# Kernel optimization log

Hardware: AMD Instinct MI355X
Metric: run time of the kernel (lower is better)

Reference implementation:

```python
import jax, jax.numpy as jnp
import numpy as np

N = 50000      # nodes
E = 800000     # edges
IN = 128       # in_channels
H = 128        # hidden_channels
OUT = 500      # out_channels
EPS = 1e-5


def setup_inputs() -> dict:
    key = jax.random.key(0)
    ks = jax.random.split(key, 8)
    def rn(k, shape, scale=0.05):
        return jax.random.normal(k, shape, jnp.float32) * scale
    return {
        "x": jax.random.normal(ks[0], (N, IN), jnp.float32),
        "edge_index": jax.random.randint(ks[1], (2, E), 0, N, dtype=jnp.int32),
        "W1": rn(ks[2], (IN, H)), "b1": jnp.zeros((H,), jnp.float32),
        "g1": jnp.ones((H,), jnp.float32), "be1": jnp.zeros((H,), jnp.float32),
        "W2": rn(ks[3], (H, 2 * H)), "b2": jnp.zeros((2 * H,), jnp.float32),
        "g2": jnp.ones((2 * H,), jnp.float32), "be2": jnp.zeros((2 * H,), jnp.float32),
        "W3": rn(ks[4], (2 * H, H)), "b3": jnp.zeros((H,), jnp.float32),
        "g3": jnp.ones((H,), jnp.float32), "be3": jnp.zeros((H,), jnp.float32),
        "Wl1": rn(ks[5], (H, H // 2)), "bl1": jnp.zeros((H // 2,), jnp.float32),
        "g4": jnp.ones((H // 2,), jnp.float32), "be4": jnp.zeros((H // 2,), jnp.float32),
        "Wl2": rn(ks[6], (H // 2, OUT)), "bl2": jnp.zeros((OUT,), jnp.float32),
    }


def layer_norm(x, g, b):
    mu = jnp.mean(x, axis=-1, keepdims=True)
    var = jnp.mean(jnp.square(x - mu), axis=-1, keepdims=True)
    return (x - mu) * jax.lax.rsqrt(var + EPS) * g + b


def gcn_conv(x, W, b, src, dst, n):
    # PyG GCNConv: x' = D^{-1/2} (A + I) D^{-1/2} (x W) + b, with self-loops.
    h = x @ W                                   # [N, F]
    ones = jnp.ones(src.shape[0], h.dtype)
    deg = jax.ops.segment_sum(ones, dst, num_segments=n) + 1.0  # +1 self-loop
    dinv = jnp.where(deg > 0, jax.lax.rsqrt(deg), 0.0)          # [N]
    coef = dinv[src] * dinv[dst]                # [E]
    agg = jax.ops.segment_sum(h[src] * coef[:, None], dst, num_segments=n)
    agg = agg + h * jnp.square(dinv)[:, None]   # self-loop messages
    return agg + b


def reference(x, edge_index, W1, b1, g1, be1, W2, b2, g2, be2,
              W3, b3, g3, be3, Wl1, bl1, g4, be4, Wl2, bl2):
    # eval mode: dropout is identity
    src, dst = edge_index[0], edge_index[1]
    n = x.shape[0]
    h = jax.nn.elu(layer_norm(gcn_conv(x, W1, b1, src, dst, n), g1, be1))
    h = jax.nn.elu(layer_norm(gcn_conv(h, W2, b2, src, dst, n), g2, be2))
    h = jax.nn.elu(layer_norm(gcn_conv(h, W3, b3, src, dst, n), g3, be3))
    h = jax.nn.elu(layer_norm(h @ Wl1 + bl1, g4, be4))
    return h @ Wl2 + bl2
```

## Files before the change

### kernel.cpp

```cpp
#include <hip/hip_runtime.h>
#include <cstdint>


#define LN_EPS 1e-5f

typedef __attribute__((ext_vector_type(8))) short bf16x8;
typedef __attribute__((ext_vector_type(4))) float f32x4;

static __device__ __forceinline__ ushort f2bf(float f) {
  union { float f; uint u; } c; c.f = f;
  uint u = c.u;
  return (ushort)((u + 0x7fffu + ((u >> 16) & 1u)) >> 16);
}
static __device__ __forceinline__ float bf2f(ushort h) {
  union { uint u; float f; } c; c.u = (uint)h << 16;
  return c.f;
}


__global__ void deg_kernel(const int* __restrict__ dst, int* __restrict__ deg, int E) {
  int e = blockIdx.x * blockDim.x + threadIdx.x;
  if (e < E) atomicAdd(&deg[dst[e]], 1);
}

__global__ void scan1_kernel(const int* __restrict__ deg, int* __restrict__ excl,
                             int* __restrict__ bsums, float* __restrict__ dinv, int N) {
  __shared__ int s[256];
  int tid = threadIdx.x;
  int i = blockIdx.x * 256 + tid;
  int v = (i < N) ? deg[i] : 0;
  s[tid] = v;
  __syncthreads();
  for (int o = 1; o < 256; o <<= 1) {
    int t = (tid >= o) ? s[tid - o] : 0;
    __syncthreads();
    if (tid >= o) s[tid] += t;
    __syncthreads();
  }
  if (i < N) {
    excl[i] = s[tid] - v;
    dinv[i] = rsqrtf((float)v + 1.0f);
  }
  if (tid == 255) bsums[blockIdx.x] = s[tid];
}

__global__ void scan23_kernel(int* __restrict__ rowptr, int* __restrict__ fill,
                              const int* __restrict__ bsums, int N, int Etotal, int nb) {
  __shared__ int sh[256];
  const int tid = threadIdx.x;
  const int bix = blockIdx.x;
  int v = (tid < bix && tid < nb) ? bsums[tid] : 0;
  sh[tid] = v;
  __syncthreads();
  for (int o = 128; o > 0; o >>= 1) {
    if (tid < o) sh[tid] += sh[tid + o];
    __syncthreads();
  }
  const int off = sh[0];
  int i = bix * 256 + tid;
  if (i < N) {
    int r = rowptr[i] + off;
    rowptr[i] = r;
    fill[i] = r;
  } else if (i == N) {
    rowptr[N] = Etotal;
  }
}

__global__ void fill_kernel(const int* __restrict__ src, const int* __restrict__ dst,
                            int* __restrict__ fill, int* __restrict__ srcs, int E) {
  int e = blockIdx.x * blockDim.x + threadIdx.x;
  if (e >= E) return;
  int idx = atomicAdd(&fill[dst[e]], 1);
  srcs[idx] = src[e];
}


struct WConvArgs {
  const float* w[5];
  ushort* wt[5];
  int K[5], N[5];
  int off[6];
};

__global__ void prep_kernel(WConvArgs a, int total, int* __restrict__ deg, int Nn) {
  int i = blockIdx.x * blockDim.x + threadIdx.x;
  if (i < Nn) deg[i] = 0;
  if (i < 768) a.wt[4][32000 + i] = 0;
  if (i >= total) return;
  int m = 0;
  while (i >= a.off[m + 1]) m++;
  int j = i - a.off[m];
  int k = j / a.N[m], n = j - k * a.N[m];
  a.wt[m][(size_t)n * a.K[m] + k] = f2bf(a.w[m][j]);
}

#define TBM 128
#define TBN 128
#define TBK 32
#define LDK 40

template <int AF32>
__global__ __launch_bounds__(256, 2) void mfma_gemm_kernel(
    const void* __restrict__ A, const ushort* __restrict__ Bt,
    const float* __restrict__ bias, ushort* __restrict__ Cout,
    int M, int N, int K) {
  __shared__ ushort As[TBM][LDK];
  __shared__ ushort Bs[TBN][LDK];
  const int tid = threadIdx.x;
  const int lane = tid & 63;
  const int w = tid >> 6;
  const int wm = w & 1, wn = w >> 1;
  const int quad = lane >> 4, l16 = lane & 15;
  const int rowBase = blockIdx.y * TBM;
  const int colBase = blockIdx.x * TBN;

  f32x4 acc[4][4] = {};
  const int lr = tid >> 2;
  const int lk = (tid & 3) * 8;

  for (int k0 = 0; k0 < K; k0 += TBK) {
#pragma unroll
    for (int h = 0; h < 2; h++) {
      int r = lr + h * 64;
      int grow = rowBase + r;
      if (AF32) {
        const float* Af = (const float*)A;
        float4 v0 = make_float4(0.f, 0.f, 0.f, 0.f), v1 = v0;
        if (grow < M) {
          const float* ap = Af + (size_t)grow * K + k0 + lk;
          v0 = *(const float4*)ap;
          v1 = *(const float4*)(ap + 4);
        }
        uint4 wv;
        wv.x = (uint)f2bf(v0.x) | ((uint)f2bf(v0.y) << 16);
        wv.y = (uint)f2bf(v0.z) | ((uint)f2bf(v0.w) << 16);
        wv.z = (uint)f2bf(v1.x) | ((uint)f2bf(v1.y) << 16);
        wv.w = (uint)f2bf(v1.z) | ((uint)f2bf(v1.w) << 16);
        *(uint4*)&As[r][lk] = wv;
      } else {
        const ushort* Ab = (const ushort*)A;
        uint4 va = make_uint4(0, 0, 0, 0);
        if (grow < M) va = *(const uint4*)(Ab + (size_t)grow * K + k0 + lk);
        *(uint4*)&As[r][lk] = va;
      }
      int gcol = colBase + r;
      uint4 vb = make_uint4(0, 0, 0, 0);
      if (gcol < N) vb = *(const uint4*)(Bt + (size_t)gcol * K + k0 + lk);
      *(uint4*)&Bs[r][lk] = vb;
    }
    __syncthreads();
    bf16x8 af[4], bfr[4];
#pragma unroll
    for (int i = 0; i < 4; i++) {
      af[i]  = *(const bf16x8*)&As[wm * 64 + i * 16 + l16][quad * 8];
      bfr[i] = *(const bf16x8*)&Bs[wn * 64 + i * 16 + l16][quad * 8];
    }
#pragma unroll
    for (int i = 0; i < 4; i++)
#pragma unroll
      for (int j = 0; j < 4; j++)
        acc[i][j] = __builtin_amdgcn_mfma_f32_16x16x32_bf16(af[i], bfr[j], acc[i][j], 0, 0, 0);
    __syncthreads();
  }
#pragma unroll
  for (int i = 0; i < 4; i++) {
    int row0 = rowBase + wm * 64 + i * 16 + quad * 4;
#pragma unroll
    for (int j = 0; j < 4; j++) {
      int col = colBase + wn * 64 + j * 16 + l16;
      if (col >= N) continue;
      float bv = bias ? bias[col] : 0.f;
#pragma unroll
      for (int r = 0; r < 4; r++) {
        int row = row0 + r;
        if (row >= M) continue;
        Cout[(size_t)row * N + col] = f2bf(acc[i][j][r] + bv);
      }
    }
  }
}

__global__ __launch_bounds__(256) void l4_kernel(
    const ushort* __restrict__ A, const ushort* __restrict__ Bt1,
    const float* __restrict__ bias1, const float* __restrict__ gamma,
    const float* __restrict__ beta, ushort* __restrict__ Hout, int M) {
  const int tid = threadIdx.x;
  const int lane = tid & 63;
  const int w = tid >> 6;
  const int quad = lane >> 4, l16 = lane & 15;
  const int rowBase = blockIdx.x * 64 + w * 16;

  bf16x8 bfr[4][4];
#pragma unroll
  for (int j = 0; j < 4; j++)
#pragma unroll
    for (int kk = 0; kk < 4; kk++)
      bfr[j][kk] = *(const bf16x8*)(Bt1 + (size_t)(j * 16 + l16) * 128 + kk * 32 + quad * 8);

  const int arow = rowBase + l16;
  bf16x8 af[4] = {};
  if (arow < M) {
#pragma unroll
    for (int kk = 0; kk < 4; kk++)
      af[kk] = *(const bf16x8*)(A + (size_t)arow * 128 + kk * 32 + quad * 8);
  }

  f32x4 acc[4] = {};
#pragma unroll
  for (int j = 0; j < 4; j++)
#pragma unroll
    for (int kk = 0; kk < 4; kk++)
      acc[j] = __builtin_amdgcn_mfma_f32_16x16x32_bf16(af[kk], bfr[j][kk], acc[j], 0, 0, 0);

#pragma unroll
  for (int r = 0; r < 4; r++) {
    float v[4];
    float s = 0.f;
#pragma unroll
    for (int j = 0; j < 4; j++) {
      v[j] = acc[j][r] + bias1[j * 16 + l16];
      s += v[j];
    }
#pragma unroll
    for (int o = 8; o >= 1; o >>= 1) s += __shfl_xor(s, o, 16);
    float mean = s * (1.0f / 64.0f);
    float q = 0.f;
#pragma unroll
    for (int j = 0; j < 4; j++) {
      float d = v[j] - mean;
      q += d * d;
    }
#pragma unroll
    for (int o = 8; o >= 1; o >>= 1) q += __shfl_xor(q, o, 16);
    float rstd = rsqrtf(q * (1.0f / 64.0f) + LN_EPS);
    int grow = rowBase + quad * 4 + r;
    if (grow < M) {
#pragma unroll
      for (int j = 0; j < 4; j++) {
        int col = j * 16 + l16;
        float y = (v[j] - mean) * rstd * gamma[col] + beta[col];
        y = (y > 0.f) ? y : expm1f(y);
        Hout[(size_t)grow * 64 + col] = f2bf(y);
      }
    }
  }
}

__global__ __launch_bounds__(256, 4) void l5_kernel(
    const ushort* __restrict__ H, const ushort* __restrict__ Bt2,
    const float* __restrict__ bias2, float* __restrict__ Cout, int M) {
  __shared__ ushort h4s[16][68];
  __shared__ __align__(16) float sout[16][500];
  const int tid = threadIdx.x;
  const int lane = tid & 63;
  const int w = tid >> 6;
  const int quad = lane >> 4, l16 = lane & 15;
  const int rowBase = blockIdx.x * 16;

  if (tid < 128) {
    int r = tid >> 3, c8 = (tid & 7) * 8;
    int grow = rowBase + r;
    uint4 v = make_uint4(0, 0, 0, 0);
    if (grow < M) v = *(const uint4*)(H + (size_t)grow * 64 + c8);
    *(uint4*)&h4s[r][c8] = v;
  }

  bf16x8 breg[8][2];
  float bvreg[8];
#pragma unroll
  for (int c = 0; c < 8; c++) {
    const int bcol = (w * 8 + c) * 16 + l16;
    breg[c][0] = *(const bf16x8*)(Bt2 + (size_t)bcol * 64 + quad * 8);
    breg[c][1] = *(const bf16x8*)(Bt2 + (size_t)bcol * 64 + 32 + quad * 8);
    bvreg[c] = (bcol < 500) ? bias2[bcol] : 0.f;
  }
  __syncthreads();

  bf16x8 a0 = *(const bf16x8*)&h4s[l16][quad * 8];
  bf16x8 a1 = *(const bf16x8*)&h4s[l16][quad * 8 + 32];
#pragma unroll
  for (int c = 0; c < 8; c++) {
    f32x4 pacc = {0.f, 0.f, 0.f, 0.f};
    pacc = __builtin_amdgcn_mfma_f32_16x16x32_bf16(a0, breg[c][0], pacc, 0, 0, 0);
    pacc = __builtin_amdgcn_mfma_f32_16x16x32_bf16(a1, breg[c][1], pacc, 0, 0, 0);
    const int col = (w * 8 + c) * 16 + l16;
    if (col < 500) {
#pragma unroll
      for (int r = 0; r < 4; r++)
        sout[quad * 4 + r][col] = pacc[r] + bvreg[c];
    }
  }
  __syncthreads();

#pragma unroll
  for (int k = 0; k < 8; k++) {
    int idx = k * 256 + tid;
    if (idx < 2000) {
      int r = idx / 125;
      int c4 = idx - r * 125;
      int grow = rowBase + r;
      if (grow < M) {
        float4 v = *(float4*)&sout[r][c4 * 4];
        *(float4*)&Cout[(size_t)grow * 500 + c4 * 4] = v;
      }
    }
  }
}


static __device__ __forceinline__ void acc8(float* a, uint4 v, float c) {
  a[0] += c * bf2f((ushort)(v.x & 0xffffu)); a[1] += c * bf2f((ushort)(v.x >> 16));
  a[2] += c * bf2f((ushort)(v.y & 0xffffu)); a[3] += c * bf2f((ushort)(v.y >> 16));
  a[4] += c * bf2f((ushort)(v.z & 0xffffu)); a[5] += c * bf2f((ushort)(v.z >> 16));
  a[6] += c * bf2f((ushort)(v.w & 0xffffu)); a[7] += c * bf2f((ushort)(v.w >> 16));
}

__global__ __launch_bounds__(256) void agg_kernel(
    const ushort* __restrict__ hb, const int* __restrict__ rowptr,
    const int* __restrict__ srcs, const float* __restrict__ dinv,
    uint* __restrict__ out, int Nn) {
  const int wave = threadIdx.x >> 6;
  const int n = blockIdx.x * 4 + wave;
  if (n >= Nn) return;
  const int lane = threadIdx.x & 63;
  const int g = lane >> 4, l16 = lane & 15;
  const uint4* h4 = (const uint4*)hb;
  const float di = dinv[n];
  float a[8] = {0.f, 0.f, 0.f, 0.f, 0.f, 0.f, 0.f, 0.f};
  if (g == 0) {
    uint4 sv = h4[(size_t)n * 16 + l16];
    acc8(a, sv, di * di);
  }
  int i = rowptr[n] + g;
  const int e = rowptr[n + 1];
  for (; i + 4 < e; i += 8) {
    int s0 = srcs[i], s1 = srcs[i + 4];
    float c0 = dinv[s0] * di, c1 = dinv[s1] * di;
    uint4 v0 = h4[(size_t)s0 * 16 + l16];
    uint4 v1 = h4[(size_t)s1 * 16 + l16];
    acc8(a, v0, c0);
    acc8(a, v1, c1);
  }
  if (i < e) {
    int s = srcs[i];
    float c = dinv[s] * di;
    uint4 v = h4[(size_t)s * 16 + l16];
    acc8(a, v, c);
  }
#pragma unroll
  for (int k = 0; k < 8; k++) {
    a[k] += __shfl_xor(a[k], 16);
    a[k] += __shfl_xor(a[k], 32);
  }
  if (g == 0) {
    uint4 o;
    o.x = (uint)f2bf(a[0]) | ((uint)f2bf(a[1]) << 16);
    o.y = (uint)f2bf(a[2]) | ((uint)f2bf(a[3]) << 16);
    o.z = (uint)f2bf(a[4]) | ((uint)f2bf(a[5]) << 16);
    o.w = (uint)f2bf(a[6]) | ((uint)f2bf(a[7]) << 16);
    ((uint4*)out)[(size_t)n * 16 + l16] = o;
  }
}

__global__ __launch_bounds__(256) void agg_ln_kernel(
    const ushort* __restrict__ hb, const int* __restrict__ rowptr,
    const int* __restrict__ srcs, const float* __restrict__ dinv,
    const float* __restrict__ bias, const float* __restrict__ gamma,
    const float* __restrict__ beta, uint* __restrict__ out, int Nn) {
  const int wave = threadIdx.x >> 6;
  const int n = blockIdx.x * 4 + wave;
  if (n >= Nn) return;
  const int lane = threadIdx.x & 63;
  const int g = lane >> 4, l16 = lane & 15;
  const uint4* h4 = (const uint4*)hb;
  const float di = dinv[n];
  float a[8] = {0.f, 0.f, 0.f, 0.f, 0.f, 0.f, 0.f, 0.f};
  if (g == 0) {
    uint4 sv = h4[(size_t)n * 16 + l16];
    acc8(a, sv, di * di);
    float4 b0 = ((const float4*)bias)[l16 * 2];
    float4 b1 = ((const float4*)bias)[l16 * 2 + 1];
    a[0] += b0.x; a[1] += b0.y; a[2] += b0.z; a[3] += b0.w;
    a[4] += b1.x; a[5] += b1.y; a[6] += b1.z; a[7] += b1.w;
  }
  int i = rowptr[n] + g;
  const int e = rowptr[n + 1];
  for (; i + 4 < e; i += 8) {
    int s0 = srcs[i], s1 = srcs[i + 4];
    float c0 = dinv[s0] * di, c1 = dinv[s1] * di;
    uint4 v0 = h4[(size_t)s0 * 16 + l16];
    uint4 v1 = h4[(size_t)s1 * 16 + l16];
    acc8(a, v0, c0);
    acc8(a, v1, c1);
  }
  if (i < e) {
    int s = srcs[i];
    float c = dinv[s] * di;
    uint4 v = h4[(size_t)s * 16 + l16];
    acc8(a, v, c);
  }
#pragma unroll
  for (int k = 0; k < 8; k++) {
    a[k] += __shfl_xor(a[k], 16);
    a[k] += __shfl_xor(a[k], 32);
  }
  float s = ((a[0] + a[1]) + (a[2] + a[3])) + ((a[4] + a[5]) + (a[6] + a[7]));
  s += __shfl_xor(s, 8);
  s += __shfl_xor(s, 4);
  s += __shfl_xor(s, 2);
  s += __shfl_xor(s, 1);
  float mean = s * (1.0f / 128.0f);
  float q = 0.f;
#pragma unroll
  for (int k = 0; k < 8; k++) {
    float d = a[k] - mean;
    q += d * d;
  }
  q += __shfl_xor(q, 8);
  q += __shfl_xor(q, 4);
  q += __shfl_xor(q, 2);
  q += __shfl_xor(q, 1);
  float rstd = rsqrtf(q * (1.0f / 128.0f) + LN_EPS);
  if (g == 0) {
    float4 g0 = ((const float4*)gamma)[l16 * 2];
    float4 g1 = ((const float4*)gamma)[l16 * 2 + 1];
    float4 e0 = ((const float4*)beta)[l16 * 2];
    float4 e1 = ((const float4*)beta)[l16 * 2 + 1];
    float gv[8] = {g0.x, g0.y, g0.z, g0.w, g1.x, g1.y, g1.z, g1.w};
    float ev[8] = {e0.x, e0.y, e0.z, e0.w, e1.x, e1.y, e1.z, e1.w};
    float y[8];
#pragma unroll
    for (int k = 0; k < 8; k++) {
      float t = (a[k] - mean) * rstd * gv[k] + ev[k];
      y[k] = (t > 0.f) ? t : expm1f(t);
    }
    uint4 o;
    o.x = (uint)f2bf(y[0]) | ((uint)f2bf(y[1]) << 16);
    o.y = (uint)f2bf(y[2]) | ((uint)f2bf(y[3]) << 16);
    o.z = (uint)f2bf(y[4]) | ((uint)f2bf(y[5]) << 16);
    o.w = (uint)f2bf(y[6]) | ((uint)f2bf(y[7]) << 16);
    ((uint4*)out)[(size_t)n * 16 + l16] = o;
  }
}

template <int F, bool IN_BF16>
__global__ __launch_bounds__(F) void ln_elu_kernel(const void* __restrict__ xin,
                                                   const float* __restrict__ g,
                                                   const float* __restrict__ be,
                                                   ushort* __restrict__ out) {
  constexpr int NW = (F + 63) / 64;
  __shared__ float sb[NW];
  const int row = blockIdx.x;
  const int f = threadIdx.x;
  float v;
  if (IN_BF16) v = bf2f(((const ushort*)xin)[(size_t)row * F + f]);
  else         v = ((const float*)xin)[(size_t)row * F + f];
  float s = v;
#pragma unroll
  for (int o = 32; o >= 1; o >>= 1) s += __shfl_xor(s, o);
  float mean;
  if constexpr (NW == 1) {
    mean = s * (1.0f / F);
  } else {
    if ((f & 63) == 0) sb[f >> 6] = s;
    __syncthreads();
    float t = 0.f;
#pragma unroll
    for (int w2 = 0; w2 < NW; w2++) t += sb[w2];
    mean = t * (1.0f / F);
    __syncthreads();
  }
  float d = v - mean;
  float q = d * d;
#pragma unroll
  for (int o = 32; o >= 1; o >>= 1) q += __shfl_xor(q, o);
  float var;
  if constexpr (NW == 1) {
    var = q * (1.0f / F);
  } else {
    if ((f & 63) == 0) sb[f >> 6] = q;
    __syncthreads();
    float t = 0.f;
#pragma unroll
    for (int w2 = 0; w2 < NW; w2++) t += sb[w2];
    var = t * (1.0f / F);
  }
  float y = d * rsqrtf(var + LN_EPS) * g[f] + be[f];
  out[(size_t)row * F + f] = f2bf((y > 0.f) ? y : expm1f(y));
}


extern "C" void kernel_launch(void* const* d_in, const int* in_sizes, int n_in,
                              void* d_out, int out_size, void* d_ws, size_t ws_size,
                              hipStream_t stream) {
  const float* x   = (const float*)d_in[0];
  const int*   ei  = (const int*)d_in[1];
  const float* W1  = (const float*)d_in[2];
  const float* b1  = (const float*)d_in[3];
  const float* g1  = (const float*)d_in[4];
  const float* be1 = (const float*)d_in[5];
  const float* W2  = (const float*)d_in[6];
  const float* b2  = (const float*)d_in[7];
  const float* g2  = (const float*)d_in[8];
  const float* be2 = (const float*)d_in[9];
  const float* W3  = (const float*)d_in[10];
  const float* b3  = (const float*)d_in[11];
  const float* g3  = (const float*)d_in[12];
  const float* be3 = (const float*)d_in[13];
  const float* Wl1 = (const float*)d_in[14];
  const float* bl1 = (const float*)d_in[15];
  const float* g4  = (const float*)d_in[16];
  const float* be4 = (const float*)d_in[17];
  const float* Wl2 = (const float*)d_in[18];
  const float* bl2 = (const float*)d_in[19];

  const int N = in_sizes[0] / 128;
  const int E = in_sizes[1] / 2;
  const int* esrc = ei;
  const int* edst = ei + E;

  char* p = (char*)d_ws;
  ushort* Pb = (ushort*)p;            p += (size_t)N * 256 * 2;
  ushort* Qb = (ushort*)p;            p += (size_t)N * 256 * 2;
  ushort* W1t = (ushort*)p;           p += 128 * 128 * 2;
  ushort* W2t = (ushort*)p;           p += 128 * 256 * 2;
  ushort* W3t = (ushort*)p;           p += 256 * 128 * 2;
  ushort* Wl1t = (ushort*)p;          p += 128 * 64 * 2;
  ushort* Wl2t = (ushort*)p;          p += 64 * 512 * 2;
  int*   srcs  = (int*)p;             p += (size_t)E * 4;
  int*   deg   = (int*)p;             p += (size_t)N * 4;
  float* dinv  = (float*)p;           p += (size_t)N * 4;
  int*   rowptr= (int*)p;             p += (size_t)(N + 2) * 4;
  int*   fill  = (int*)p;             p += (size_t)N * 4;
  int*   bsums = (int*)p;             p += 256 * 4;

  const int nb = (N + 255) / 256;
  const int eb = (E + 255) / 256;

  WConvArgs wa;
  wa.w[0] = W1;  wa.wt[0] = W1t;  wa.K[0] = 128; wa.N[0] = 128;
  wa.w[1] = W2;  wa.wt[1] = W2t;  wa.K[1] = 128; wa.N[1] = 256;
  wa.w[2] = W3;  wa.wt[2] = W3t;  wa.K[2] = 256; wa.N[2] = 128;
  wa.w[3] = Wl1; wa.wt[3] = Wl1t; wa.K[3] = 128; wa.N[3] = 64;
  wa.w[4] = Wl2; wa.wt[4] = Wl2t; wa.K[4] = 64;  wa.N[4] = 500;
  wa.off[0] = 0;
  for (int m = 0; m < 5; m++) wa.off[m + 1] = wa.off[m] + wa.K[m] * wa.N[m];
  int wtotal = wa.off[5];
  int ptotal = wtotal > N ? wtotal : N;
  prep_kernel<<<(ptotal + 255) / 256, 256, 0, stream>>>(wa, wtotal, deg, N);

  deg_kernel<<<eb, 256, 0, stream>>>(edst, deg, E);
  scan1_kernel<<<nb, 256, 0, stream>>>(deg, rowptr, bsums, dinv, N);
  scan23_kernel<<<(N + 256) / 256, 256, 0, stream>>>(rowptr, fill, bsums, N, E, nb);
  fill_kernel<<<eb, 256, 0, stream>>>(esrc, edst, fill, srcs, E);

  const int ab = (N + 3) / 4;
  auto grid_of = [&](int M, int Nn) {
    return dim3((Nn + TBN - 1) / TBN, (M + TBM - 1) / TBM);
  };

  mfma_gemm_kernel<1><<<grid_of(N, 128), 256, 0, stream>>>(
      x, W1t, nullptr, Pb, N, 128, 128);
  agg_ln_kernel<<<ab, 256, 0, stream>>>(Pb, rowptr, srcs, dinv, b1, g1, be1, (uint*)Qb, N);

  agg_kernel<<<ab, 256, 0, stream>>>(Qb, rowptr, srcs, dinv, (uint*)Pb, N);
  mfma_gemm_kernel<0><<<grid_of(N, 256), 256, 0, stream>>>(
      Pb, W2t, b2, Qb, N, 256, 128);
  ln_elu_kernel<256, true><<<N, 256, 0, stream>>>(Qb, g2, be2, Pb);

  mfma_gemm_kernel<0><<<grid_of(N, 128), 256, 0, stream>>>(
      Pb, W3t, nullptr, Qb, N, 128, 256);
  agg_ln_kernel<<<ab, 256, 0, stream>>>(Qb, rowptr, srcs, dinv, b3, g3, be3, (uint*)Pb, N);

  l4_kernel<<<dim3((N + 63) / 64), 256, 0, stream>>>(
      Pb, Wl1t, bl1, g4, be4, Qb, N);

  l5_kernel<<<dim3((N + 15) / 16), 256, 0, stream>>>(
      Qb, Wl2t, bl2, (float*)d_out, N);
}
```

Before: 510.7 us.

## Fuse final linear+LN+ELU layer with output projection kernel

Merges the l4 (128->64 linear, layernorm, ELU) and l5 (64->500 projection) kernels into one kernel that keeps the 64-row intermediate in shared memory. The intermediate no longer round-trips through global memory and one launch is removed. Each block now processes 64 rows in four 16-row sub-tiles with extra barriers. The larger shared footprint and fewer blocks may reduce occupancy for the output-store phase.

```diff
diff --git a/kernel.cpp b/kernel.cpp
--- a/kernel.cpp
+++ b/kernel.cpp
@@ -181,89 +181,71 @@
   }
 }
 
-__global__ __launch_bounds__(256) void l4_kernel(
+__global__ __launch_bounds__(256) void l45_kernel(
     const ushort* __restrict__ A, const ushort* __restrict__ Bt1,
     const float* __restrict__ bias1, const float* __restrict__ gamma,
-    const float* __restrict__ beta, ushort* __restrict__ Hout, int M) {
-  const int tid = threadIdx.x;
-  const int lane = tid & 63;
-  const int w = tid >> 6;
-  const int quad = lane >> 4, l16 = lane & 15;
-  const int rowBase = blockIdx.x * 64 + w * 16;
-
-  bf16x8 bfr[4][4];
-#pragma unroll
-  for (int j = 0; j < 4; j++)
-#pragma unroll
-    for (int kk = 0; kk < 4; kk++)
-      bfr[j][kk] = *(const bf16x8*)(Bt1 + (size_t)(j * 16 + l16) * 128 + kk * 32 + quad * 8);
-
-  const int arow = rowBase + l16;
-  bf16x8 af[4] = {};
-  if (arow < M) {
-#pragma unroll
-    for (int kk = 0; kk < 4; kk++)
-      af[kk] = *(const bf16x8*)(A + (size_t)arow * 128 + kk * 32 + quad * 8);
-  }
-
-  f32x4 acc[4] = {};
-#pragma unroll
-  for (int j = 0; j < 4; j++)
-#pragma unroll
-    for (int kk = 0; kk < 4; kk++)
-      acc[j] = __builtin_amdgcn_mfma_f32_16x16x32_bf16(af[kk], bfr[j][kk], acc[j], 0, 0, 0);
-
-#pragma unroll
-  for (int r = 0; r < 4; r++) {
-    float v[4];
-    float s = 0.f;
-#pragma unroll
-    for (int j = 0; j < 4; j++) {
-      v[j] = acc[j][r] + bias1[j * 16 + l16];
-      s += v[j];
-    }
-#pragma unroll
-    for (int o = 8; o >= 1; o >>= 1) s += __shfl_xor(s, o, 16);
-    float mean = s * (1.0f / 64.0f);
-    float q = 0.f;
-#pragma unroll
-    for (int j = 0; j < 4; j++) {
-      float d = v[j] - mean;
-      q += d * d;
-    }
-#pragma unroll
-    for (int o = 8; o >= 1; o >>= 1) q += __shfl_xor(q, o, 16);
-    float rstd = rsqrtf(q * (1.0f / 64.0f) + LN_EPS);
-    int grow = rowBase + quad * 4 + r;
-    if (grow < M) {
-#pragma unroll
-      for (int j = 0; j < 4; j++) {
-        int col = j * 16 + l16;
-        float y = (v[j] - mean) * rstd * gamma[col] + beta[col];
-        y = (y > 0.f) ? y : expm1f(y);
-        Hout[(size_t)grow * 64 + col] = f2bf(y);
-      }
-    }
-  }
-}
-
-__global__ __launch_bounds__(256, 4) void l5_kernel(
-    const ushort* __restrict__ H, const ushort* __restrict__ Bt2,
+    const float* __restrict__ beta, const ushort* __restrict__ Bt2,
     const float* __restrict__ bias2, float* __restrict__ Cout, int M) {
-  __shared__ ushort h4s[16][68];
+  __shared__ ushort h4s[64][68];
   __shared__ __align__(16) float sout[16][500];
   const int tid = threadIdx.x;
   const int lane = tid & 63;
   const int w = tid >> 6;
   const int quad = lane >> 4, l16 = lane & 15;
-  const int rowBase = blockIdx.x * 16;
-
-  if (tid < 128) {
-    int r = tid >> 3, c8 = (tid & 7) * 8;
-    int grow = rowBase + r;
-    uint4 v = make_uint4(0, 0, 0, 0);
-    if (grow < M) v = *(const uint4*)(H + (size_t)grow * 64 + c8);
-    *(uint4*)&h4s[r][c8] = v;
+  const int rowBase = blockIdx.x * 64;
+  const int waveRow = rowBase + w * 16;
+
+  bf16x8 bfr1[4][4];
+#pragma unroll
+  for (int j = 0; j < 4; j++)
+#pragma unroll
+    for (int kk = 0; kk < 4; kk++)
+      bfr1[j][kk] = *(const bf16x8*)(Bt1 + (size_t)(j * 16 + l16) * 128 + kk * 32 + quad * 8);
+
+  const int arow = waveRow + l16;
+  bf16x8 af[4] = {};
+  if (arow < M) {
+#pragma unroll
+    for (int kk = 0; kk < 4; kk++)
+      af[kk] = *(const bf16x8*)(A + (size_t)arow * 128 + kk * 32 + quad * 8);
+  }
+
+  f32x4 acc1[4] = {};
+#pragma unroll
+  for (int j = 0; j < 4; j++)
+#pragma unroll
+    for (int kk = 0; kk < 4; kk++)
+      acc1[j] = __builtin_amdgcn_mfma_f32_16x16x32_bf16(af[kk], bfr1[j][kk], acc1[j], 0, 0, 0);
+
+#pragma unroll
+  for (int r = 0; r < 4; r++) {
+    float v[4];
+    float s = 0.f;
+#pragma unroll
+    for (int j = 0; j < 4; j++) {
+      v[j] = acc1[j][r] + bias1[j * 16 + l16];
+      s += v[j];
+    }
+#pragma unroll
+    for (int o = 8; o >= 1; o >>= 1) s += __shfl_xor(s, o, 16);
+    float mean = s * (1.0f / 64.0f);
+    float q = 0.f;
+#pragma unroll
+    for (int j = 0; j < 4; j++) {
+      float d = v[j] - mean;
+      q += d * d;
+    }
+#pragma unroll
+    for (int o = 8; o >= 1; o >>= 1) q += __shfl_xor(q, o, 16);
+    float rstd = rsqrtf(q * (1.0f / 64.0f) + LN_EPS);
+    int lrow = w * 16 + quad * 4 + r;
+#pragma unroll
+    for (int j = 0; j < 4; j++) {
+      int col = j * 16 + l16;
+      float y = (v[j] - mean) * rstd * gamma[col] + beta[col];
+      y = (y > 0.f) ? y : expm1f(y);
+      h4s[lrow][col] = f2bf(y);
+    }
   }
 
   bf16x8 breg[8][2];
@@ -277,34 +259,37 @@
   }
   __syncthreads();
 
-  bf16x8 a0 = *(const bf16x8*)&h4s[l16][quad * 8];
-  bf16x8 a1 = *(const bf16x8*)&h4s[l16][quad * 8 + 32];
-#pragma unroll
-  for (int c = 0; c < 8; c++) {
-    f32x4 pacc = {0.f, 0.f, 0.f, 0.f};
-    pacc = __builtin_amdgcn_mfma_f32_16x16x32_bf16(a0, breg[c][0], pacc, 0, 0, 0);
-    pacc = __builtin_amdgcn_mfma_f32_16x16x32_bf16(a1, breg[c][1], pacc, 0, 0, 0);
-    const int col = (w * 8 + c) * 16 + l16;
-    if (col < 500) {
-#pragma unroll
-      for (int r = 0; r < 4; r++)
-        sout[quad * 4 + r][col] = pacc[r] + bvreg[c];
-    }
-  }
-  __syncthreads();
-
-#pragma unroll
-  for (int k = 0; k < 8; k++) {
-    int idx = k * 256 + tid;
-    if (idx < 2000) {
-      int r = idx / 125;
-      int c4 = idx - r * 125;
-      int grow = rowBase + r;
-      if (grow < M) {
-        float4 v = *(float4*)&sout[r][c4 * 4];
-        *(float4*)&Cout[(size_t)grow * 500 + c4 * 4] = v;
+#pragma unroll 1
+  for (int rt = 0; rt < 4; rt++) {
+    bf16x8 a0 = *(const bf16x8*)&h4s[rt * 16 + l16][quad * 8];
+    bf16x8 a1 = *(const bf16x8*)&h4s[rt * 16 + l16][quad * 8 + 32];
+#pragma unroll
+    for (int c = 0; c < 8; c++) {
+      f32x4 pacc = {0.f, 0.f, 0.f, 0.f};
+      pacc = __builtin_amdgcn_mfma_f32_16x16x32_bf16(a0, breg[c][0], pacc, 0, 0, 0);
+      pacc = __builtin_amdgcn_mfma_f32_16x16x32_bf16(a1, breg[c][1], pacc, 0, 0, 0);
+      const int col = (w * 8 + c) * 16 + l16;
+      if (col < 500) {
+#pragma unroll
+        for (int r = 0; r < 4; r++)
+          sout[quad * 4 + r][col] = pacc[r] + bvreg[c];
       }
     }
+    __syncthreads();
+#pragma unroll
+    for (int k = 0; k < 8; k++) {
+      int idx = k * 256 + tid;
+      if (idx < 2000) {
+        int r = idx / 125;
+        int c4 = idx - r * 125;
+        int grow = rowBase + rt * 16 + r;
+        if (grow < M) {
+          float4 v = *(float4*)&sout[r][c4 * 4];
+          *(float4*)&Cout[(size_t)grow * 500 + c4 * 4] = v;
+        }
+      }
+    }
+    __syncthreads();
   }
 }
 
@@ -573,9 +558,6 @@
       Pb, W3t, nullptr, Qb, N, 128, 256);
   agg_ln_kernel<<<ab, 256, 0, stream>>>(Qb, rowptr, srcs, dinv, b3, g3, be3, (uint*)Pb, N);
 
-  l4_kernel<<<dim3((N + 63) / 64), 256, 0, stream>>>(
-      Pb, Wl1t, bl1, g4, be4, Qb, N);
-
-  l5_kernel<<<dim3((N + 15) / 16), 256, 0, stream>>>(
-      Qb, Wl2t, bl2, (float*)d_out, N);
-}
+  l45_kernel<<<dim3((N + 63) / 64), 256, 0, stream>>>(
+      Pb, Wl1t, bl1, g4, be4, Wl2t, bl2, (float*)d_out, N);
+}
```

Result: faster. 497.1 us (-2.7%).
